# Optimization experiments

Measured on AMD Instinct MI355X. Metric: run time of the kernel, lower is better.

Reference implementation:

```python
import jax, jax.numpy as jnp
import numpy as np
import math

B, N, D, H = 4, 2048, 512, 8
DK = D // H


def setup_inputs() -> dict:
    key = jax.random.key(0)
    ks = jax.random.split(key, 7)
    s = 1.0 / math.sqrt(D)
    return {
        "Q": jax.random.normal(ks[0], (B, N, D), jnp.float32),
        "K": jax.random.normal(ks[1], (B, N, D), jnp.float32),
        "V": jax.random.normal(ks[2], (B, N, D), jnp.float32),
        "Wq": jax.random.normal(ks[3], (D, D), jnp.float32) * s,
        "bq": jax.random.normal(ks[4], (D,), jnp.float32) * s,
        "Wo": jax.random.normal(ks[5], (D, D), jnp.float32) * s,
        "bo": jax.random.normal(ks[6], (D,), jnp.float32) * s,
    }


def _split_heads(x):
    b, n, _ = x.shape
    return x.reshape(b, n, H, DK).transpose(0, 2, 1, 3)  # [B,H,N,dk]


def reference(Q, K, V, Wq, bq, Wo, bo):
    # Faithful to source: W_q projects Q, K, AND V (source bug kept).
    proj = lambda x: jnp.einsum("bnd,ed->bne", x, Wq) + bq
    q = _split_heads(proj(Q))
    k = _split_heads(proj(K))
    v = _split_heads(proj(V))
    scores = jnp.einsum("bhnd,bhmd->bhnm", q, k) / math.sqrt(DK)  # [B,H,N,N]
    # Faithful to source: softmax over dim=1 == the HEADS axis.
    probs = jax.nn.softmax(scores, axis=1)
    A = jnp.einsum("bhnm,bhmd->bhnd", probs, v)  # [B,H,N,dk]
    A = A.transpose(0, 2, 1, 3).reshape(B, N, D)  # combine heads
    return jnp.einsum("bnd,ed->bne", A, Wo) + bo
```

## Files before the change

kernel.cpp:

```cpp
#include <hip/hip_runtime.h>
#include <hip/hip_bf16.h>

#define B_  4
#define N_  2048
#define D_  512
#define H_  8

typedef unsigned short u16;
typedef __attribute__((ext_vector_type(8))) unsigned short ushort8;
typedef __attribute__((ext_vector_type(4))) unsigned short us4;
typedef __attribute__((ext_vector_type(8))) short short8;
typedef __attribute__((ext_vector_type(4))) float float4v;

__device__ __forceinline__ float bf2f(u16 u) {
    union { unsigned int i; float f; } v;
    v.i = ((unsigned int)u) << 16;
    return v.f;
}
__device__ __forceinline__ u16 f2bf(float f) {
    union { float f; unsigned int i; } v;
    v.f = f;
    unsigned int r = v.i + 0x7FFFu + ((v.i >> 16) & 1u);
    return (u16)(r >> 16);
}
__device__ __forceinline__ u16 f2bf_fast(float f) {
    union { float f; unsigned int i; } v;
    v.f = f;
    return (u16)((v.i + 0x8000u) >> 16);
}

__device__ __forceinline__ void gload_lds16(const void* g, void* l) {
    __builtin_amdgcn_global_load_lds(
        (const __attribute__((address_space(1))) unsigned int*)g,
        (__attribute__((address_space(3))) unsigned int*)l, 16, 0, 0);
}

#define WAIT_VM(N) do { \
    asm volatile("s_waitcnt vmcnt(" #N ")" ::: "memory"); \
    __builtin_amdgcn_sched_barrier(0); } while (0)
#define WAIT_LGKM0 do { \
    asm volatile("s_waitcnt lgkmcnt(0)" ::: "memory"); \
    __builtin_amdgcn_sched_barrier(0); } while (0)
#define BARRIER do { \
    __builtin_amdgcn_s_barrier(); \
    __builtin_amdgcn_sched_barrier(0); } while (0)

__global__ __launch_bounds__(256) void wconv(
    const float* __restrict__ Wq, const float* __restrict__ Wo,
    u16* __restrict__ out)
{
    const int idx = (blockIdx.x * 256 + threadIdx.x) * 8;
    const float* src = blockIdx.y ? Wo : Wq;
    u16* dst = out + (size_t)blockIdx.y * (D_ * D_) + idx;
    float4v a = *(const float4v*)(src + idx);
    float4v b = *(const float4v*)(src + idx + 4);
    ushort8 o;
    #pragma unroll
    for (int j = 0; j < 4; ++j) { o[j] = f2bf(a[j]); o[j + 4] = f2bf(b[j]); }
    *(ushort8*)dst = o;
}

__global__ __launch_bounds__(256) void cvt3(
    const float* __restrict__ Q, const float* __restrict__ K,
    const float* __restrict__ V, u16* __restrict__ out)
{
    const size_t NBD = (size_t)B_ * N_ * D_;
    const float* src = (blockIdx.y == 0) ? Q : ((blockIdx.y == 1) ? K : V);
    u16* dst = out + (size_t)blockIdx.y * NBD;
    size_t idx = ((size_t)blockIdx.x * 256 + threadIdx.x) * 8;
    float4v a = *(const float4v*)(src + idx);
    float4v b = *(const float4v*)(src + idx + 4);
    ushort8 o;
    #pragma unroll
    for (int j = 0; j < 4; ++j) { o[j] = f2bf(a[j]); o[j + 4] = f2bf(b[j]); }
    *(ushort8*)(dst + idx) = o;
}

template <int INK, bool WB16, bool OUTB16, int NZ>
__global__ __launch_bounds__(256) void proj_mfma(
    const void* __restrict__ X0v, const void* __restrict__ X1v,
    const void* __restrict__ X2v, const void* __restrict__ Wv,
    const float* __restrict__ bias, void* __restrict__ C0v, int M)
{
    __shared__ u16 As[128][32];
    __shared__ u16 Bs[128][32];

    const int t = threadIdx.x;
    const int flat = blockIdx.x;
    const int xcd = flat & 7, rr = flat >> 3;
    const int eb = rr & 3, g = rr >> 2;
    const int zm = xcd + 8 * g;
    const int z  = zm >> 6;
    const int e0 = eb * 128;
    const int m0 = (zm & 63) * 128;

    const void* Xv = (z == 0) ? X0v : ((z == 1) ? X1v : X2v);
    const int w = t >> 6, l = t & 63;
    const int lane16 = l & 15, quad = l >> 4;
    const int wr = (w >> 1) * 64;
    const int wc = (w & 1) * 64;

    float4v acc[4][4];
    #pragma unroll
    for (int i = 0; i < 4; ++i)
        #pragma unroll
        for (int j = 0; j < 4; ++j)
            acc[i][j] = (float4v){0.f, 0.f, 0.f, 0.f};

    for (int k0 = 0; k0 < 512; k0 += 32) {
        __syncthreads();

        if (INK == 1) {
            const u16* X = (const u16*)Xv;
            #pragma unroll
            for (int i = 0; i < 2; ++i) {
                int r0 = w * 32 + i * 16;
                gload_lds16(X + (size_t)(m0 + r0 + (l >> 2)) * 512 + k0 + (l & 3) * 8,
                            &As[r0][0]);
            }
        } else if (INK == 0) {
            const float* X = (const float*)Xv;
            #pragma unroll
            for (int i = 0; i < 2; ++i) {
                int v   = t + 256 * i;
                int row = v >> 2;
                int c8  = (v & 3) * 8;
                const float* xp = X + (size_t)(m0 + row) * 512 + k0 + c8;
                float4v x0 = *(const float4v*)xp;
                float4v x1 = *(const float4v*)(xp + 4);
                ushort8 o;
                #pragma unroll
                for (int j = 0; j < 4; ++j) {
                    o[j]     = f2bf_fast(x0[j]);
                    o[j + 4] = f2bf_fast(x1[j]);
                }
                *(ushort8*)&As[row][c8] = o;
            }
        } else {
            const u16* P0 = (const u16*)X0v;
            const u16* P1 = (const u16*)X1v;
            #pragma unroll
            for (int i = 0; i < 2; ++i) {
                int v   = t + 256 * i;
                int row = v >> 2;
                int c8  = (v & 3) * 8;
                size_t gi = (size_t)(m0 + row) * 512 + k0 + c8;
                ushort8 a = *(const ushort8*)(P0 + gi);
                ushort8 b = *(const ushort8*)(P1 + gi);
                ushort8 o;
                #pragma unroll
                for (int j = 0; j < 8; ++j) o[j] = f2bf(bf2f(a[j]) + bf2f(b[j]));
                *(ushort8*)&As[row][c8] = o;
            }
        }

        if (WB16) {
            const u16* Wb = (const u16*)Wv;
            #pragma unroll
            for (int i = 0; i < 2; ++i) {
                int r0 = w * 32 + i * 16;
                gload_lds16(Wb + (size_t)(e0 + r0 + (l >> 2)) * 512 + k0 + (l & 3) * 8,
                            &Bs[r0][0]);
            }
        } else {
            const float* W = (const float*)Wv;
            #pragma unroll
            for (int i = 0; i < 2; ++i) {
                int v   = t + 256 * i;
                int row = v >> 2;
                int c8  = (v & 3) * 8;
                const float* wp = W + (size_t)(e0 + row) * 512 + k0 + c8;
                float4v w0 = *(const float4v*)wp;
                float4v w1 = *(const float4v*)(wp + 4);
                ushort8 o;
                #pragma unroll
                for (int j = 0; j < 4; ++j) {
                    o[j]     = f2bf_fast(w0[j]);
                    o[j + 4] = f2bf_fast(w1[j]);
                }
                *(ushort8*)&Bs[row][c8] = o;
            }
        }
        __syncthreads();

        short8 af[4], bfr[4];
        #pragma unroll
        for (int i = 0; i < 4; ++i)
            af[i] = *(const short8*)&As[wr + i * 16 + lane16][quad * 8];
        #pragma unroll
        for (int j = 0; j < 4; ++j)
            bfr[j] = *(const short8*)&Bs[wc + j * 16 + lane16][quad * 8];
        #pragma unroll
        for (int i = 0; i < 4; ++i)
            #pragma unroll
            for (int j = 0; j < 4; ++j)
                acc[i][j] = __builtin_amdgcn_mfma_f32_16x16x32_bf16(
                    af[i], bfr[j], acc[i][j], 0, 0, 0);
    }

    float bj[4];
    #pragma unroll
    for (int j = 0; j < 4; ++j) bj[j] = bias[e0 + wc + j * 16 + lane16];

    if (OUTB16) {
        if (z == 2) {
            u16* C = (u16*)C0v + 2 * (size_t)M * D_;
            #pragma unroll
            for (int i = 0; i < 4; ++i) {
                int mrow = m0 + wr + i * 16 + quad * 4;
                int bb = mrow >> 11, nb = mrow & (N_ - 1);
                #pragma unroll
                for (int j = 0; j < 4; ++j) {
                    int e = e0 + wc + j * 16 + lane16;
                    us4 o;
                    #pragma unroll
                    for (int r = 0; r < 4; ++r) o[r] = f2bf(acc[i][j][r] + bj[j]);
                    *(us4*)(C + (size_t)(bb * D_ + e) * N_ + nb) = o;
                }
            }
        } else {
            u16* C = (u16*)C0v + (size_t)z * (size_t)M * D_;
            #pragma unroll
            for (int i = 0; i < 4; ++i)
                #pragma unroll
                for (int j = 0; j < 4; ++j) {
                    int e = e0 + wc + j * 16 + lane16;
                    #pragma unroll
                    for (int r = 0; r < 4; ++r) {
                        int mrow = m0 + wr + i * 16 + quad * 4 + r;
                        C[(size_t)mrow * D_ + e] = f2bf(acc[i][j][r] + bj[j]);
                    }
                }
        }
    } else {
        float* C = (float*)C0v;
        #pragma unroll
        for (int i = 0; i < 4; ++i)
            #pragma unroll
            for (int j = 0; j < 4; ++j) {
                int e = e0 + wc + j * 16 + lane16;
                #pragma unroll
                for (int r = 0; r < 4; ++r) {
                    int mrow = m0 + wr + i * 16 + quad * 4 + r;
                    C[(size_t)mrow * D_ + e] = acc[i][j][r] + bj[j];
                }
            }
    }
}

__global__ __launch_bounds__(512, 2) void attn_mfma6(
    const u16* __restrict__ Qp, const u16* __restrict__ Kp,
    const u16* __restrict__ Vpt, u16* __restrict__ A0)
{
    __shared__ u16 Ks[2][32][520];
    __shared__ u16 Vs[512][36];
    __shared__ u16 Ps[4][8][16][36];

    const int t = threadIdx.x;
    const int w = t >> 6, l = t & 63;
    const int lane16 = l & 15, quad = l >> 4;
    const int ns = w >> 1, ms = w & 1;

    const int flat = blockIdx.x;
    const int xcd  = flat & 7;
    const int b = xcd >> 1;
    const int z = xcd & 1;
    const int n0 = (flat >> 3) * 64 + ns * 16;
    const int seg  = N_ / 2;
    const int mbeg = z * seg;
    u16* A = A0 + (size_t)z * ((size_t)B_ * N_ * D_);

    const u16* Kb = Kp + (size_t)b * N_ * D_;
    const int vd0 = t >> 2, vpart = (t & 3) * 8;
    const u16* Vsrc = Vpt + (size_t)(b * D_) * N_ + vpart;

    short8 qfrag[8][2];
    {
        const u16* qb = Qp + ((size_t)(b * N_ + n0 + lane16) * D_ + quad * 8);
        #pragma unroll
        for (int h = 0; h < 8; ++h)
            #pragma unroll
            for (int dc = 0; dc < 2; ++dc)
                qfrag[h][dc] = *(const short8*)(qb + h * 64 + dc * 32);
    }

    float4v aacc[8][2];
    #pragma unroll
    for (int h = 0; h < 8; ++h)
        #pragma unroll
        for (int dt = 0; dt < 2; ++dt)
            aacc[h][dt] = (float4v){0.f, 0.f, 0.f, 0.f};

    ushort8 vreg[4];
    const int nch = seg / 32;

    #pragma unroll
    for (int i = 0; i < 4; ++i)
        gload_lds16(Kb + (size_t)(mbeg + w * 4 + i) * D_ + l * 8,
                    &Ks[0][w * 4 + i][0]);
    #pragma unroll
    for (int i = 0; i < 4; ++i)
        vreg[i] = *(const ushort8*)(Vsrc + (size_t)(i * 128 + vd0) * N_ + mbeg);
    #pragma unroll
    for (int i = 0; i < 4; ++i)
        gload_lds16(Kb + (size_t)(mbeg + 32 + w * 4 + i) * D_ + l * 8,
                    &Ks[1][w * 4 + i][0]);
    WAIT_VM(8);
    BARRIER;

    for (int c = 0; c < nch; ++c) {
        const int cur = c & 1;
        const int mc  = mbeg + c * 32;

        if (c < nch - 1) { WAIT_VM(4); } else { WAIT_VM(0); }

        #pragma unroll
        for (int i = 0; i < 4; ++i)
            *(ushort8*)&Vs[i * 128 + vd0][vpart] = vreg[i];

        float4v sacc[8];
        #pragma unroll
        for (int h = 0; h < 8; ++h) sacc[h] = (float4v){0.f, 0.f, 0.f, 0.f};
        __builtin_amdgcn_s_setprio(1);
        #pragma unroll
        for (int h = 0; h < 8; ++h)
            #pragma unroll
            for (int dc = 0; dc < 2; ++dc) {
                short8 kf = *(const short8*)
                    &Ks[cur][ms * 16 + lane16][h * 64 + dc * 32 + quad * 8];
                sacc[h] = __builtin_amdgcn_mfma_f32_16x16x32_bf16(
                    qfrag[h][dc], kf, sacc[h], 0, 0, 0);
            }
        __builtin_amdgcn_s_setprio(0);

        #pragma unroll
        for (int r = 0; r < 4; ++r) {
            float p[8]; float sum = 0.f;
            #pragma unroll
            for (int h = 0; h < 8; ++h) {
                p[h] = __expf(sacc[h][r] * 0.125f);
                sum += p[h];
            }
            float inv = __builtin_amdgcn_rcpf(sum);
            #pragma unroll
            for (int h = 0; h < 8; ++h)
                Ps[ns][h][quad * 4 + r][ms * 16 + lane16] = f2bf(p[h] * inv);
        }

        if (c + 1 < nch) {
            #pragma unroll
            for (int i = 0; i < 4; ++i)
                vreg[i] = *(const ushort8*)
                    (Vsrc + (size_t)(i * 128 + vd0) * N_ + mc + 32);
        }

        WAIT_LGKM0;
        BARRIER;

        if (c + 2 < nch) {
            #pragma unroll
            for (int i = 0; i < 4; ++i)
                gload_lds16(Kb + (size_t)(mc + 64 + w * 4 + i) * D_ + l * 8,
                            &Ks[cur][w * 4 + i][0]);
        }

        __builtin_amdgcn_s_setprio(1);
        #pragma unroll
        for (int h = 0; h < 8; ++h) {
            short8 pf = *(const short8*)&Ps[ns][h][lane16][quad * 8];
            #pragma unroll
            for (int dt = 0; dt < 2; ++dt) {
                short8 vf = *(const short8*)
                    &Vs[h * 64 + (ms * 2 + dt) * 16 + lane16][quad * 8];
                aacc[h][dt] = __builtin_amdgcn_mfma_f32_16x16x32_bf16(
                    pf, vf, aacc[h][dt], 0, 0, 0);
            }
        }
        __builtin_amdgcn_s_setprio(0);

        if (c < nch - 1) {
            if (c + 2 < nch) { WAIT_VM(8); } else { WAIT_VM(4); }
            WAIT_LGKM0;
            BARRIER;
        }
    }

    #pragma unroll
    for (int h = 0; h < 8; ++h)
        #pragma unroll
        for (int dt = 0; dt < 2; ++dt)
            #pragma unroll
            for (int r = 0; r < 4; ++r) {
                const int n = n0 + quad * 4 + r;
                const int d = h * 64 + (ms * 2 + dt) * 16 + lane16;
                A[(size_t)(b * N_ + n) * D_ + d] = f2bf(aacc[h][dt][r]);
            }
}

extern "C" void kernel_launch(void* const* d_in, const int* in_sizes, int n_in,
                              void* d_out, int out_size, void* d_ws, size_t ws_size,
                              hipStream_t stream)
{
    const float* Q  = (const float*)d_in[0];
    const float* K  = (const float*)d_in[1];
    const float* V  = (const float*)d_in[2];
    const float* Wq = (const float*)d_in[3];
    const float* bq = (const float*)d_in[4];
    const float* Wo = (const float*)d_in[5];
    const float* bo = (const float*)d_in[6];
    float* out = (float*)d_out;
    u16*   ws  = (u16*)d_ws;

    const size_t NBD = (size_t)B_ * N_ * D_;
    const int M = B_ * N_;

    const size_t need6 = (6 * NBD + 2 * (size_t)D_ * D_) * sizeof(u16);

    if (ws_size >= need6) {
        u16* S0 = ws;
        u16* S1 = ws + NBD;
        u16* S2 = ws + 2 * NBD;
        u16* S3 = ws + 3 * NBD;
        u16* Wb = ws + 6 * NBD;

        cvt3<<<dim3((unsigned)(NBD / 2048), 3), dim3(256), 0, stream>>>(Q, K, V, S0);
        wconv<<<dim3(128, 2), dim3(256), 0, stream>>>(Wq, Wo, Wb);

        proj_mfma<1, true, true, 3><<<dim3(768), dim3(256), 0, stream>>>(
            S0, S1, S2, Wb, bq, S3, M);

        attn_mfma6<<<dim3(256), dim3(512), 0, stream>>>(
            S3, S3 + NBD, S3 + 2 * NBD, S0);

        proj_mfma<2, true, false, 1><<<dim3(256), dim3(256), 0, stream>>>(
            S0, S1, S1, Wb + (size_t)D_ * D_, bo, out, M);
    } else {
        u16* Qp  = ws;
        u16* Kp  = ws + NBD;
        u16* Vpt = ws + 2 * NBD;
        u16* Pa  = ws + 3 * NBD;
        u16* Pb  = ws + 4 * NBD;
        u16* Wb  = ws + 5 * NBD;

        wconv<<<dim3(128, 2), dim3(256), 0, stream>>>(Wq, Wo, Wb);

        proj_mfma<0, true, true, 3><<<dim3(768), dim3(256), 0, stream>>>(
            Q, K, V, Wb, bq, Qp, M);

        attn_mfma6<<<dim3(256), dim3(512), 0, stream>>>(Qp, Kp, Vpt, Pa);

        proj_mfma<2, true, false, 1><<<dim3(256), dim3(256), 0, stream>>>(
            Pa, Pb, Pb, Wb + (size_t)D_ * D_, bo, out, M);
    }
}
```

Measured before the change: 241.3 us.

## Split attention heads across twice the waves and fuse weight conversion into input cast

```diff
diff --git a/kernel.cpp b/kernel.cpp
--- a/kernel.cpp
+++ b/kernel.cpp
@@ -60,13 +60,30 @@
     *(ushort8*)dst = o;
 }
 
-__global__ __launch_bounds__(256) void cvt3(
+__global__ __launch_bounds__(256) void cvt4(
     const float* __restrict__ Q, const float* __restrict__ K,
-    const float* __restrict__ V, u16* __restrict__ out)
+    const float* __restrict__ V, const float* __restrict__ Wq,
+    const float* __restrict__ Wo, u16* __restrict__ out,
+    u16* __restrict__ wb)
 {
+    const int y = blockIdx.y;
+    if (y == 3) {
+        if (blockIdx.x >= 256) return;
+        const int idx = (blockIdx.x * 256 + threadIdx.x) * 8;
+        const bool hi = idx >= D_ * D_;
+        const float* src = hi ? Wo : Wq;
+        const int off = hi ? idx - D_ * D_ : idx;
+        float4v a = *(const float4v*)(src + off);
+        float4v b = *(const float4v*)(src + off + 4);
+        ushort8 o;
+        #pragma unroll
+        for (int j = 0; j < 4; ++j) { o[j] = f2bf(a[j]); o[j + 4] = f2bf(b[j]); }
+        *(ushort8*)(wb + idx) = o;
+        return;
+    }
     const size_t NBD = (size_t)B_ * N_ * D_;
-    const float* src = (blockIdx.y == 0) ? Q : ((blockIdx.y == 1) ? K : V);
-    u16* dst = out + (size_t)blockIdx.y * NBD;
+    const float* src = (y == 0) ? Q : ((y == 1) ? K : V);
+    u16* dst = out + (size_t)y * NBD;
     size_t idx = ((size_t)blockIdx.x * 256 + threadIdx.x) * 8;
     float4v a = *(const float4v*)(src + idx);
     float4v b = *(const float4v*)(src + idx + 4);
@@ -248,18 +265,19 @@
     }
 }
 
-__global__ __launch_bounds__(512, 2) void attn_mfma6(
+__global__ __launch_bounds__(1024, 4) void attn_mfma7(
     const u16* __restrict__ Qp, const u16* __restrict__ Kp,
     const u16* __restrict__ Vpt, u16* __restrict__ A0)
 {
     __shared__ u16 Ks[2][32][520];
     __shared__ u16 Vs[512][36];
     __shared__ u16 Ps[4][8][16][36];
+    __shared__ float Sx[4][2][16][16][2];
 
     const int t = threadIdx.x;
     const int w = t >> 6, l = t & 63;
     const int lane16 = l & 15, quad = l >> 4;
-    const int ns = w >> 1, ms = w & 1;
+    const int ns = w >> 2, ms = (w >> 1) & 1, hs = w & 1;
 
     const int flat = blockIdx.x;
     const int xcd  = flat & 7;
@@ -271,116 +289,122 @@
     u16* A = A0 + (size_t)z * ((size_t)B_ * N_ * D_);
 
     const u16* Kb = Kp + (size_t)b * N_ * D_;
-    const int vd0 = t >> 2, vpart = (t & 3) * 8;
-    const u16* Vsrc = Vpt + (size_t)(b * D_) * N_ + vpart;
-
-    short8 qfrag[8][2];
+    const int vd = t >> 2, vpart = (t & 3) * 8;
+    const u16* Vsrc = Vpt + ((size_t)(b * D_ + vd)) * N_ + vpart;
+    const int dt = ms * 2 + hs;
+
+    short8 qfrag[4][2];
     {
         const u16* qb = Qp + ((size_t)(b * N_ + n0 + lane16) * D_ + quad * 8);
         #pragma unroll
-        for (int h = 0; h < 8; ++h)
+        for (int hh = 0; hh < 4; ++hh)
             #pragma unroll
             for (int dc = 0; dc < 2; ++dc)
-                qfrag[h][dc] = *(const short8*)(qb + h * 64 + dc * 32);
-    }
-
-    float4v aacc[8][2];
-    #pragma unroll
-    for (int h = 0; h < 8; ++h)
-        #pragma unroll
-        for (int dt = 0; dt < 2; ++dt)
-            aacc[h][dt] = (float4v){0.f, 0.f, 0.f, 0.f};
-
-    ushort8 vreg[4];
+                qfrag[hh][dc] = *(const short8*)(qb + (hs * 4 + hh) * 64 + dc * 32);
+    }
+
+    float4v aacc[8];
+    #pragma unroll
+    for (int h = 0; h < 8; ++h) aacc[h] = (float4v){0.f, 0.f, 0.f, 0.f};
+
+    ushort8 vreg[2];
     const int nch = seg / 32;
 
     #pragma unroll
-    for (int i = 0; i < 4; ++i)
-        gload_lds16(Kb + (size_t)(mbeg + w * 4 + i) * D_ + l * 8,
-                    &Ks[0][w * 4 + i][0]);
-    #pragma unroll
-    for (int i = 0; i < 4; ++i)
-        vreg[i] = *(const ushort8*)(Vsrc + (size_t)(i * 128 + vd0) * N_ + mbeg);
-    #pragma unroll
-    for (int i = 0; i < 4; ++i)
-        gload_lds16(Kb + (size_t)(mbeg + 32 + w * 4 + i) * D_ + l * 8,
-                    &Ks[1][w * 4 + i][0]);
-    WAIT_VM(8);
+    for (int i = 0; i < 2; ++i)
+        gload_lds16(Kb + (size_t)(mbeg + w * 2 + i) * D_ + l * 8,
+                    &Ks[0][w * 2 + i][0]);
+    #pragma unroll
+    for (int i = 0; i < 2; ++i)
+        vreg[i] = *(const ushort8*)(Vsrc + (size_t)(i * 256) * N_ + mbeg);
+    #pragma unroll
+    for (int i = 0; i < 2; ++i)
+        gload_lds16(Kb + (size_t)(mbeg + 32 + w * 2 + i) * D_ + l * 8,
+                    &Ks[1][w * 2 + i][0]);
+    WAIT_VM(4);
     BARRIER;
 
     for (int c = 0; c < nch; ++c) {
         const int cur = c & 1;
         const int mc  = mbeg + c * 32;
 
-        if (c < nch - 1) { WAIT_VM(4); } else { WAIT_VM(0); }
-
-        #pragma unroll
-        for (int i = 0; i < 4; ++i)
-            *(ushort8*)&Vs[i * 128 + vd0][vpart] = vreg[i];
-
-        float4v sacc[8];
-        #pragma unroll
-        for (int h = 0; h < 8; ++h) sacc[h] = (float4v){0.f, 0.f, 0.f, 0.f};
+        if (c + 1 < nch) { WAIT_VM(2); } else { WAIT_VM(0); }
+
+        #pragma unroll
+        for (int i = 0; i < 2; ++i)
+            *(ushort8*)&Vs[i * 256 + vd][vpart] = vreg[i];
+
+        float4v sacc[4];
+        #pragma unroll
+        for (int hh = 0; hh < 4; ++hh) sacc[hh] = (float4v){0.f, 0.f, 0.f, 0.f};
         __builtin_amdgcn_s_setprio(1);
         #pragma unroll
-        for (int h = 0; h < 8; ++h)
+        for (int hh = 0; hh < 4; ++hh)
             #pragma unroll
             for (int dc = 0; dc < 2; ++dc) {
                 short8 kf = *(const short8*)
-                    &Ks[cur][ms * 16 + lane16][h * 64 + dc * 32 + quad * 8];
-                sacc[h] = __builtin_amdgcn_mfma_f32_16x16x32_bf16(
-                    qfrag[h][dc], kf, sacc[h], 0, 0, 0);
+                    &Ks[cur][ms * 16 + lane16][(hs * 4 + hh) * 64 + dc * 32 + quad * 8];
+                sacc[hh] = __builtin_amdgcn_mfma_f32_16x16x32_bf16(
+                    qfrag[hh][dc], kf, sacc[hh], 0, 0, 0);
             }
         __builtin_amdgcn_s_setprio(0);
 
+        float psum[4];
         #pragma unroll
         for (int r = 0; r < 4; ++r) {
-            float p[8]; float sum = 0.f;
-            #pragma unroll
-            for (int h = 0; h < 8; ++h) {
-                p[h] = __expf(sacc[h][r] * 0.125f);
-                sum += p[h];
-            }
-            float inv = __builtin_amdgcn_rcpf(sum);
-            #pragma unroll
-            for (int h = 0; h < 8; ++h)
-                Ps[ns][h][quad * 4 + r][ms * 16 + lane16] = f2bf(p[h] * inv);
+            float s = 0.f;
+            #pragma unroll
+            for (int hh = 0; hh < 4; ++hh) {
+                sacc[hh][r] = __expf(sacc[hh][r] * 0.125f);
+                s += sacc[hh][r];
+            }
+            psum[r] = s;
+            Sx[ns][ms][quad * 4 + r][lane16][hs] = s;
         }
 
         if (c + 1 < nch) {
             #pragma unroll
-            for (int i = 0; i < 4; ++i)
+            for (int i = 0; i < 2; ++i)
                 vreg[i] = *(const ushort8*)
-                    (Vsrc + (size_t)(i * 128 + vd0) * N_ + mc + 32);
+                    (Vsrc + (size_t)(i * 256) * N_ + mc + 32);
         }
 
         WAIT_LGKM0;
         BARRIER;
 
+        #pragma unroll
+        for (int r = 0; r < 4; ++r) {
+            float other = Sx[ns][ms][quad * 4 + r][lane16][hs ^ 1];
+            float inv = __builtin_amdgcn_rcpf(psum[r] + other);
+            #pragma unroll
+            for (int hh = 0; hh < 4; ++hh)
+                Ps[ns][hs * 4 + hh][quad * 4 + r][ms * 16 + lane16] =
+                    f2bf_fast(sacc[hh][r] * inv);
+        }
+
         if (c + 2 < nch) {
             #pragma unroll
-            for (int i = 0; i < 4; ++i)
-                gload_lds16(Kb + (size_t)(mc + 64 + w * 4 + i) * D_ + l * 8,
-                            &Ks[cur][w * 4 + i][0]);
-        }
+            for (int i = 0; i < 2; ++i)
+                gload_lds16(Kb + (size_t)(mc + 64 + w * 2 + i) * D_ + l * 8,
+                            &Ks[cur][w * 2 + i][0]);
+        }
+
+        WAIT_LGKM0;
+        BARRIER;
 
         __builtin_amdgcn_s_setprio(1);
         #pragma unroll
         for (int h = 0; h < 8; ++h) {
             short8 pf = *(const short8*)&Ps[ns][h][lane16][quad * 8];
-            #pragma unroll
-            for (int dt = 0; dt < 2; ++dt) {
-                short8 vf = *(const short8*)
-                    &Vs[h * 64 + (ms * 2 + dt) * 16 + lane16][quad * 8];
-                aacc[h][dt] = __builtin_amdgcn_mfma_f32_16x16x32_bf16(
-                    pf, vf, aacc[h][dt], 0, 0, 0);
-            }
+            short8 vf = *(const short8*)
+                &Vs[h * 64 + dt * 16 + lane16][quad * 8];
+            aacc[h] = __builtin_amdgcn_mfma_f32_16x16x32_bf16(
+                pf, vf, aacc[h], 0, 0, 0);
         }
         __builtin_amdgcn_s_setprio(0);
 
-        if (c < nch - 1) {
-            if (c + 2 < nch) { WAIT_VM(8); } else { WAIT_VM(4); }
-            WAIT_LGKM0;
+        if (c + 1 < nch) {
+            if (c + 2 < nch) { WAIT_VM(4); } else { WAIT_VM(2); }
             BARRIER;
         }
     }
@@ -388,13 +412,11 @@
     #pragma unroll
     for (int h = 0; h < 8; ++h)
         #pragma unroll
-        for (int dt = 0; dt < 2; ++dt)
-            #pragma unroll
-            for (int r = 0; r < 4; ++r) {
-                const int n = n0 + quad * 4 + r;
-                const int d = h * 64 + (ms * 2 + dt) * 16 + lane16;
-                A[(size_t)(b * N_ + n) * D_ + d] = f2bf(aacc[h][dt][r]);
-            }
+        for (int r = 0; r < 4; ++r) {
+            const int n = n0 + quad * 4 + r;
+            const int d = h * 64 + dt * 16 + lane16;
+            A[(size_t)(b * N_ + n) * D_ + d] = f2bf(aacc[h][r]);
+        }
 }
 
 extern "C" void kernel_launch(void* const* d_in, const int* in_sizes, int n_in,
@@ -423,13 +445,13 @@
         u16* S3 = ws + 3 * NBD;
         u16* Wb = ws + 6 * NBD;
 
-        cvt3<<<dim3((unsigned)(NBD / 2048), 3), dim3(256), 0, stream>>>(Q, K, V, S0);
-        wconv<<<dim3(128, 2), dim3(256), 0, stream>>>(Wq, Wo, Wb);
+        cvt4<<<dim3((unsigned)(NBD / 2048), 4), dim3(256), 0, stream>>>(
+            Q, K, V, Wq, Wo, S0, Wb);
 
         proj_mfma<1, true, true, 3><<<dim3(768), dim3(256), 0, stream>>>(
             S0, S1, S2, Wb, bq, S3, M);
 
-        attn_mfma6<<<dim3(256), dim3(512), 0, stream>>>(
+        attn_mfma7<<<dim3(256), dim3(1024), 0, stream>>>(
             S3, S3 + NBD, S3 + 2 * NBD, S0);
 
         proj_mfma<2, true, false, 1><<<dim3(256), dim3(256), 0, stream>>>(
@@ -447,7 +469,7 @@
         proj_mfma<0, true, true, 3><<<dim3(768), dim3(256), 0, stream>>>(
             Q, K, V, Wb, bq, Qp, M);
 
-        attn_mfma6<<<dim3(256), dim3(512), 0, stream>>>(Qp, Kp, Vpt, Pa);
+        attn_mfma7<<<dim3(256), dim3(1024), 0, stream>>>(Qp, Kp, Vpt, Pa);
 
         proj_mfma<2, true, false, 1><<<dim3(256), dim3(256), 0, stream>>>(
             Pa, Pb, Pb, Wb + (size_t)D_ * D_, bo, out, M);
```

After: 243.9 us. Within noise of the previous version (+1.1%).

## Drop separate input conversion pass, retile output projection, use fast bf16 rounding

Applied to the files above, without the earlier changes.

```diff
diff --git a/kernel.cpp b/kernel.cpp
--- a/kernel.cpp
+++ b/kernel.cpp
@@ -60,27 +60,10 @@
     *(ushort8*)dst = o;
 }
 
-__global__ __launch_bounds__(256) void cvt3(
-    const float* __restrict__ Q, const float* __restrict__ K,
-    const float* __restrict__ V, u16* __restrict__ out)
-{
-    const size_t NBD = (size_t)B_ * N_ * D_;
-    const float* src = (blockIdx.y == 0) ? Q : ((blockIdx.y == 1) ? K : V);
-    u16* dst = out + (size_t)blockIdx.y * NBD;
-    size_t idx = ((size_t)blockIdx.x * 256 + threadIdx.x) * 8;
-    float4v a = *(const float4v*)(src + idx);
-    float4v b = *(const float4v*)(src + idx + 4);
-    ushort8 o;
-    #pragma unroll
-    for (int j = 0; j < 4; ++j) { o[j] = f2bf(a[j]); o[j + 4] = f2bf(b[j]); }
-    *(ushort8*)(dst + idx) = o;
-}
-
-template <int INK, bool WB16, bool OUTB16, int NZ>
-__global__ __launch_bounds__(256) void proj_mfma(
-    const void* __restrict__ X0v, const void* __restrict__ X1v,
-    const void* __restrict__ X2v, const void* __restrict__ Wv,
-    const float* __restrict__ bias, void* __restrict__ C0v, int M)
+__global__ __launch_bounds__(256) void proj1_mfma(
+    const float* __restrict__ X0, const float* __restrict__ X1,
+    const float* __restrict__ X2, const u16* __restrict__ Wb,
+    const float* __restrict__ bias, u16* __restrict__ C0)
 {
     __shared__ u16 As[128][32];
     __shared__ u16 Bs[128][32];
@@ -94,7 +77,7 @@
     const int e0 = eb * 128;
     const int m0 = (zm & 63) * 128;
 
-    const void* Xv = (z == 0) ? X0v : ((z == 1) ? X1v : X2v);
+    const float* X = (z == 0) ? X0 : ((z == 1) ? X1 : X2);
     const int w = t >> 6, l = t & 63;
     const int lane16 = l & 15, quad = l >> 4;
     const int wr = (w >> 1) * 64;
@@ -110,76 +93,28 @@
     for (int k0 = 0; k0 < 512; k0 += 32) {
         __syncthreads();
 
-        if (INK == 1) {
-            const u16* X = (const u16*)Xv;
-            #pragma unroll
-            for (int i = 0; i < 2; ++i) {
-                int r0 = w * 32 + i * 16;
-                gload_lds16(X + (size_t)(m0 + r0 + (l >> 2)) * 512 + k0 + (l & 3) * 8,
-                            &As[r0][0]);
-            }
-        } else if (INK == 0) {
-            const float* X = (const float*)Xv;
-            #pragma unroll
-            for (int i = 0; i < 2; ++i) {
-                int v   = t + 256 * i;
-                int row = v >> 2;
-                int c8  = (v & 3) * 8;
-                const float* xp = X + (size_t)(m0 + row) * 512 + k0 + c8;
-                float4v x0 = *(const float4v*)xp;
-                float4v x1 = *(const float4v*)(xp + 4);
-                ushort8 o;
-                #pragma unroll
-                for (int j = 0; j < 4; ++j) {
-                    o[j]     = f2bf_fast(x0[j]);
-                    o[j + 4] = f2bf_fast(x1[j]);
-                }
-                *(ushort8*)&As[row][c8] = o;
-            }
-        } else {
-            const u16* P0 = (const u16*)X0v;
-            const u16* P1 = (const u16*)X1v;
-            #pragma unroll
-            for (int i = 0; i < 2; ++i) {
-                int v   = t + 256 * i;
-                int row = v >> 2;
-                int c8  = (v & 3) * 8;
-                size_t gi = (size_t)(m0 + row) * 512 + k0 + c8;
-                ushort8 a = *(const ushort8*)(P0 + gi);
-                ushort8 b = *(const ushort8*)(P1 + gi);
-                ushort8 o;
-                #pragma unroll
-                for (int j = 0; j < 8; ++j) o[j] = f2bf(bf2f(a[j]) + bf2f(b[j]));
-                *(ushort8*)&As[row][c8] = o;
-            }
-        }
-
-        if (WB16) {
-            const u16* Wb = (const u16*)Wv;
-            #pragma unroll
-            for (int i = 0; i < 2; ++i) {
-                int r0 = w * 32 + i * 16;
-                gload_lds16(Wb + (size_t)(e0 + r0 + (l >> 2)) * 512 + k0 + (l & 3) * 8,
-                            &Bs[r0][0]);
-            }
-        } else {
-            const float* W = (const float*)Wv;
-            #pragma unroll
-            for (int i = 0; i < 2; ++i) {
-                int v   = t + 256 * i;
-                int row = v >> 2;
-                int c8  = (v & 3) * 8;
-                const float* wp = W + (size_t)(e0 + row) * 512 + k0 + c8;
-                float4v w0 = *(const float4v*)wp;
-                float4v w1 = *(const float4v*)(wp + 4);
-                ushort8 o;
-                #pragma unroll
-                for (int j = 0; j < 4; ++j) {
-                    o[j]     = f2bf_fast(w0[j]);
-                    o[j + 4] = f2bf_fast(w1[j]);
-                }
-                *(ushort8*)&Bs[row][c8] = o;
-            }
+        #pragma unroll
+        for (int i = 0; i < 2; ++i) {
+            int v   = t + 256 * i;
+            int row = v >> 2;
+            int c8  = (v & 3) * 8;
+            const float* xp = X + (size_t)(m0 + row) * 512 + k0 + c8;
+            float4v x0 = *(const float4v*)xp;
+            float4v x1 = *(const float4v*)(xp + 4);
+            ushort8 o;
+            #pragma unroll
+            for (int j = 0; j < 4; ++j) {
+                o[j]     = f2bf_fast(x0[j]);
+                o[j + 4] = f2bf_fast(x1[j]);
+            }
+            *(ushort8*)&As[row][c8] = o;
+        }
+
+        #pragma unroll
+        for (int i = 0; i < 2; ++i) {
+            int r0 = w * 32 + i * 16;
+            gload_lds16(Wb + (size_t)(e0 + r0 + (l >> 2)) * 512 + k0 + (l & 3) * 8,
+                        &Bs[r0][0]);
         }
         __syncthreads();
 
@@ -202,38 +137,23 @@
     #pragma unroll
     for (int j = 0; j < 4; ++j) bj[j] = bias[e0 + wc + j * 16 + lane16];
 
-    if (OUTB16) {
-        if (z == 2) {
-            u16* C = (u16*)C0v + 2 * (size_t)M * D_;
-            #pragma unroll
-            for (int i = 0; i < 4; ++i) {
-                int mrow = m0 + wr + i * 16 + quad * 4;
-                int bb = mrow >> 11, nb = mrow & (N_ - 1);
+    if (z == 2) {
+        u16* C = C0 + 2 * (size_t)B_ * N_ * D_;
+        #pragma unroll
+        for (int i = 0; i < 4; ++i) {
+            int mrow = m0 + wr + i * 16 + quad * 4;
+            int bb = mrow >> 11, nb = mrow & (N_ - 1);
+            #pragma unroll
+            for (int j = 0; j < 4; ++j) {
+                int e = e0 + wc + j * 16 + lane16;
+                us4 o;
                 #pragma unroll
-                for (int j = 0; j < 4; ++j) {
-                    int e = e0 + wc + j * 16 + lane16;
-                    us4 o;
-                    #pragma unroll
-                    for (int r = 0; r < 4; ++r) o[r] = f2bf(acc[i][j][r] + bj[j]);
-                    *(us4*)(C + (size_t)(bb * D_ + e) * N_ + nb) = o;
-                }
-            }
-        } else {
-            u16* C = (u16*)C0v + (size_t)z * (size_t)M * D_;
-            #pragma unroll
-            for (int i = 0; i < 4; ++i)
-                #pragma unroll
-                for (int j = 0; j < 4; ++j) {
-                    int e = e0 + wc + j * 16 + lane16;
-                    #pragma unroll
-                    for (int r = 0; r < 4; ++r) {
-                        int mrow = m0 + wr + i * 16 + quad * 4 + r;
-                        C[(size_t)mrow * D_ + e] = f2bf(acc[i][j][r] + bj[j]);
-                    }
-                }
+                for (int r = 0; r < 4; ++r) o[r] = f2bf(acc[i][j][r] + bj[j]);
+                *(us4*)(C + (size_t)(bb * D_ + e) * N_ + nb) = o;
+            }
         }
     } else {
-        float* C = (float*)C0v;
+        u16* C = C0 + (size_t)z * (size_t)B_ * N_ * D_;
         #pragma unroll
         for (int i = 0; i < 4; ++i)
             #pragma unroll
@@ -242,10 +162,90 @@
                 #pragma unroll
                 for (int r = 0; r < 4; ++r) {
                     int mrow = m0 + wr + i * 16 + quad * 4 + r;
-                    C[(size_t)mrow * D_ + e] = acc[i][j][r] + bj[j];
+                    C[(size_t)mrow * D_ + e] = f2bf(acc[i][j][r] + bj[j]);
                 }
             }
     }
+}
+
+__global__ __launch_bounds__(256) void proj2_mfma(
+    const u16* __restrict__ P0, const u16* __restrict__ P1,
+    const u16* __restrict__ Wv, const float* __restrict__ bias,
+    float* __restrict__ C)
+{
+    __shared__ u16 As[128][32];
+    __shared__ u16 Bs[64][32];
+
+    const int t = threadIdx.x;
+    const int flat = blockIdx.x;
+    const int xcd = flat & 7, rr = flat >> 3;
+    const int eb = rr & 7, g = rr >> 3;
+    const int m0 = (xcd + 8 * g) * 128;
+    const int e0 = eb * 64;
+
+    const int w = t >> 6, l = t & 63;
+    const int lane16 = l & 15, quad = l >> 4;
+    const int wr = (w >> 1) * 64;
+    const int wc = (w & 1) * 32;
+
+    float4v acc[4][2];
+    #pragma unroll
+    for (int i = 0; i < 4; ++i)
+        #pragma unroll
+        for (int j = 0; j < 2; ++j)
+            acc[i][j] = (float4v){0.f, 0.f, 0.f, 0.f};
+
+    for (int k0 = 0; k0 < 512; k0 += 32) {
+        __syncthreads();
+
+        #pragma unroll
+        for (int i = 0; i < 2; ++i) {
+            int v   = t + 256 * i;
+            int row = v >> 2;
+            int c8  = (v & 3) * 8;
+            size_t gi = (size_t)(m0 + row) * 512 + k0 + c8;
+            ushort8 a = *(const ushort8*)(P0 + gi);
+            ushort8 b = *(const ushort8*)(P1 + gi);
+            ushort8 o;
+            #pragma unroll
+            for (int j = 0; j < 8; ++j) o[j] = f2bf(bf2f(a[j]) + bf2f(b[j]));
+            *(ushort8*)&As[row][c8] = o;
+        }
+
+        gload_lds16(Wv + (size_t)(e0 + w * 16 + (l >> 2)) * 512 + k0 + (l & 3) * 8,
+                    &Bs[w * 16][0]);
+        __syncthreads();
+
+        short8 af[4], bfr[2];
+        #pragma unroll
+        for (int i = 0; i < 4; ++i)
+            af[i] = *(const short8*)&As[wr + i * 16 + lane16][quad * 8];
+        #pragma unroll
+        for (int j = 0; j < 2; ++j)
+            bfr[j] = *(const short8*)&Bs[wc + j * 16 + lane16][quad * 8];
+        #pragma unroll
+        for (int i = 0; i < 4; ++i)
+            #pragma unroll
+            for (int j = 0; j < 2; ++j)
+                acc[i][j] = __builtin_amdgcn_mfma_f32_16x16x32_bf16(
+                    af[i], bfr[j], acc[i][j], 0, 0, 0);
+    }
+
+    float bj[2];
+    #pragma unroll
+    for (int j = 0; j < 2; ++j) bj[j] = bias[e0 + wc + j * 16 + lane16];
+
+    #pragma unroll
+    for (int i = 0; i < 4; ++i)
+        #pragma unroll
+        for (int j = 0; j < 2; ++j) {
+            int e = e0 + wc + j * 16 + lane16;
+            #pragma unroll
+            for (int r = 0; r < 4; ++r) {
+                int mrow = m0 + wr + i * 16 + quad * 4 + r;
+                C[(size_t)mrow * D_ + e] = acc[i][j][r] + bj[j];
+            }
+        }
 }
 
 __global__ __launch_bounds__(512, 2) void attn_mfma6(
@@ -344,7 +344,7 @@
             float inv = __builtin_amdgcn_rcpf(sum);
             #pragma unroll
             for (int h = 0; h < 8; ++h)
-                Ps[ns][h][quad * 4 + r][ms * 16 + lane16] = f2bf(p[h] * inv);
+                Ps[ns][h][quad * 4 + r][ms * 16 + lane16] = f2bf_fast(p[h] * inv);
         }
 
         if (c + 1 < nch) {
@@ -412,44 +412,21 @@
     u16*   ws  = (u16*)d_ws;
 
     const size_t NBD = (size_t)B_ * N_ * D_;
-    const int M = B_ * N_;
-
-    const size_t need6 = (6 * NBD + 2 * (size_t)D_ * D_) * sizeof(u16);
-
-    if (ws_size >= need6) {
-        u16* S0 = ws;
-        u16* S1 = ws + NBD;
-        u16* S2 = ws + 2 * NBD;
-        u16* S3 = ws + 3 * NBD;
-        u16* Wb = ws + 6 * NBD;
-
-        cvt3<<<dim3((unsigned)(NBD / 2048), 3), dim3(256), 0, stream>>>(Q, K, V, S0);
-        wconv<<<dim3(128, 2), dim3(256), 0, stream>>>(Wq, Wo, Wb);
-
-        proj_mfma<1, true, true, 3><<<dim3(768), dim3(256), 0, stream>>>(
-            S0, S1, S2, Wb, bq, S3, M);
-
-        attn_mfma6<<<dim3(256), dim3(512), 0, stream>>>(
-            S3, S3 + NBD, S3 + 2 * NBD, S0);
-
-        proj_mfma<2, true, false, 1><<<dim3(256), dim3(256), 0, stream>>>(
-            S0, S1, S1, Wb + (size_t)D_ * D_, bo, out, M);
-    } else {
-        u16* Qp  = ws;
-        u16* Kp  = ws + NBD;
-        u16* Vpt = ws + 2 * NBD;
-        u16* Pa  = ws + 3 * NBD;
-        u16* Pb  = ws + 4 * NBD;
-        u16* Wb  = ws + 5 * NBD;
-
-        wconv<<<dim3(128, 2), dim3(256), 0, stream>>>(Wq, Wo, Wb);
-
-        proj_mfma<0, true, true, 3><<<dim3(768), dim3(256), 0, stream>>>(
-            Q, K, V, Wb, bq, Qp, M);
-
-        attn_mfma6<<<dim3(256), dim3(512), 0, stream>>>(Qp, Kp, Vpt, Pa);
-
-        proj_mfma<2, true, false, 1><<<dim3(256), dim3(256), 0, stream>>>(
-            Pa, Pb, Pb, Wb + (size_t)D_ * D_, bo, out, M);
-    }
-}
+
+    u16* Qp  = ws;
+    u16* Kp  = ws + NBD;
+    u16* Vpt = ws + 2 * NBD;
+    u16* Pa  = ws + 3 * NBD;
+    u16* Pb  = ws + 4 * NBD;
+    u16* Wb  = ws + 5 * NBD;
+
+    wconv<<<dim3(128, 2), dim3(256), 0, stream>>>(Wq, Wo, Wb);
+
+    proj1_mfma<<<dim3(768), dim3(256), 0, stream>>>(
+        Q, K, V, Wb, bq, Qp);
+
+    attn_mfma6<<<dim3(256), dim3(512), 0, stream>>>(Qp, Kp, Vpt, Pa);
+
+    proj2_mfma<<<dim3(512), dim3(256), 0, stream>>>(
+        Pa, Pb, Wb + (size_t)D_ * D_, bo, out);
+}
```

New measurement: 240.6 us. No clear change (-0.3%).
